# Performance work log

Hardware: AMD Instinct MI355X
Metric: run time of the kernel (lower is better)

Reference implementation:

```python
import jax, jax.numpy as jnp
import numpy as np

N_NODES = 100000
N_EDGES = 3200000
D = 256


def setup_inputs() -> dict:
    key = jax.random.key(0)
    ks = jax.random.split(key, 8)
    ego_embeddings = jax.random.normal(ks[0], (N_NODES, D), dtype=jnp.float32) * 0.1
    edge_vals = jax.random.uniform(ks[1], (N_EDGES,), dtype=jnp.float32) / 32.0  # ~normalized adjacency
    W1 = jax.random.normal(ks[2], (D, D), dtype=jnp.float32) * (1.0 / np.sqrt(D))
    b1 = jnp.zeros((D,), dtype=jnp.float32)
    W2 = jax.random.normal(ks[3], (D, D), dtype=jnp.float32) * (1.0 / np.sqrt(D))
    b2 = jnp.zeros((D,), dtype=jnp.float32)
    edge_rows = jax.random.randint(ks[4], (N_EDGES,), 0, N_NODES, dtype=jnp.int32)
    edge_cols = jax.random.randint(ks[5], (N_EDGES,), 0, N_NODES, dtype=jnp.int32)
    return {"ego_embeddings": ego_embeddings, "edge_vals": edge_vals,
            "W1": W1, "b1": b1, "W2": W2, "b2": b2,
            "edge_rows": edge_rows, "edge_cols": edge_cols}


def reference(ego_embeddings, edge_vals, W1, b1, W2, b2, edge_rows, edge_cols):
    # SpMM: side = A_in @ ego  (A_in in COO: rows, cols, vals)
    n = ego_embeddings.shape[0]
    gathered = ego_embeddings[edge_cols] * edge_vals[:, None]      # [E, D]
    side = jax.ops.segment_sum(gathered, edge_rows, num_segments=n)  # [N, D]
    # bi-interaction aggregator
    sum_emb = jax.nn.leaky_relu((ego_embeddings + side) @ W1.T + b1, negative_slope=0.01)
    bi_emb = jax.nn.leaky_relu((ego_embeddings * side) @ W2.T + b2, negative_slope=0.01)
    # dropout p=0.0 -> identity
    return sum_emb + bi_emb
```

## Files before the change

kernel.cpp:

```cpp
#include <hip/hip_runtime.h>
#include <hip/hip_fp16.h>
#include <stdint.h>

#define D 256
#define CHSH 13

typedef __attribute__((ext_vector_type(8))) short short8;
typedef __attribute__((ext_vector_type(4))) float floatx4;

__device__ __forceinline__ ushort f2bf(float f) {
    union { float f; uint32_t u; } v; v.f = f;
    uint32_t u = v.u;
    u += 0x7fffu + ((u >> 16) & 1u);
    return (ushort)(u >> 16);
}
__device__ __forceinline__ float bf2f(ushort h) {
    union { uint32_t u; float f; } v; v.u = ((uint32_t)h) << 16;
    return v.f;
}


__global__ void k_hist(const int* __restrict__ er, const int* __restrict__ ec,
                       const float* __restrict__ ev,
                       int* __restrict__ bp, uint64_t* __restrict__ aux,
                       int E, int NCH) {
    int e = blockIdx.x * 256 + threadIdx.x;
    if (e >= E) return;
    int row = er[e];
    int col = ec[e];
    int b = row * NCH + (col >> CHSH);
    atomicAdd(&bp[b], 1);
    ushort hb = __half_as_ushort(__float2half_rn(ev[e]));
    uint32_t payload = ((uint32_t)col << 15) | (uint32_t)hb;
    aux[e] = ((uint64_t)(uint32_t)b << 32) | payload;
}

__global__ void k_red(const int* __restrict__ bp, int* __restrict__ part, int nb) {
    __shared__ int s[256];
    int t = threadIdx.x;
    int base = blockIdx.x * 1024 + t * 4;
    int v = 0;
#pragma unroll
    for (int j = 0; j < 4; ++j) if (base + j < nb) v += bp[base + j];
    s[t] = v; __syncthreads();
    for (int off = 128; off; off >>= 1) {
        if (t < off) s[t] += s[t + off];
        __syncthreads();
    }
    if (t == 0) part[blockIdx.x] = s[0];
}

__global__ __launch_bounds__(1024) void k_scanpart(int* __restrict__ part, int np) {
    __shared__ int s[1024];
    int t = threadIdx.x;
    int p0 = (2 * t < np) ? part[2 * t] : 0;
    int p1 = (2 * t + 1 < np) ? part[2 * t + 1] : 0;
    int v = p0 + p1;
    s[t] = v; __syncthreads();
    for (int off = 1; off < 1024; off <<= 1) {
        int x = (t >= off) ? s[t - off] : 0;
        __syncthreads();
        s[t] += x;
        __syncthreads();
    }
    int excl = s[t] - v;
    if (2 * t < np) part[2 * t] = excl;
    if (2 * t + 1 < np) part[2 * t + 1] = excl + p0;
}

__global__ void k_scan3(int* __restrict__ bp, const int* __restrict__ part, int nb) {
    __shared__ int s[256];
    int t = threadIdx.x;
    int base = blockIdx.x * 1024 + t * 4;
    int d0 = 0, d1 = 0, d2 = 0, d3 = 0;
    if (base     < nb) d0 = bp[base];
    if (base + 1 < nb) d1 = bp[base + 1];
    if (base + 2 < nb) d2 = bp[base + 2];
    if (base + 3 < nb) d3 = bp[base + 3];
    int sum = d0 + d1 + d2 + d3;
    s[t] = sum; __syncthreads();
    for (int off = 1; off < 256; off <<= 1) {
        int x = (t >= off) ? s[t - off] : 0;
        __syncthreads();
        s[t] += x;
        __syncthreads();
    }
    int run = part[blockIdx.x] + s[t] - sum;
    if (base     < nb) bp[base]     = run; run += d0;
    if (base + 1 < nb) bp[base + 1] = run; run += d1;
    if (base + 2 < nb) bp[base + 2] = run; run += d2;
    if (base + 3 < nb) bp[base + 3] = run;
}

__global__ void k_scatter(const uint64_t* __restrict__ aux,
                          int* __restrict__ bp, uint32_t* __restrict__ csr,
                          int E, int BW) {
    int xcd = blockIdx.x & 7;
    int j = blockIdx.x >> 3;
    int e = j * 256 + threadIdx.x;
    if (e >= E) return;
    uint64_t a = aux[e];
    int b = (int)(a >> 32);
    int lo = xcd * BW;
    if (b < lo || b >= lo + BW) return;
    int p = atomicAdd(&bp[b], 1);
    csr[p] = (uint32_t)a;
}

__global__ void k_cvt(const float4* __restrict__ ego, ushort4* __restrict__ ego_bf,
                      const float4* __restrict__ W1, const float4* __restrict__ W2,
                      ushort4* __restrict__ W1b, ushort4* __restrict__ W2b, int n4) {
    int i = blockIdx.x * 256 + threadIdx.x;
    const float4* src;
    ushort4* dst;
    if (i < n4) { src = ego + i; dst = ego_bf + i; }
    else {
        int j = i - n4;
        if (j >= 32768) return;
        int k = j & 16383;
        src = ((j < 16384) ? W1 : W2) + k;
        dst = ((j < 16384) ? W1b : W2b) + k;
    }
    float4 f = *src;
    ushort4 u;
    u.x = f2bf(f.x); u.y = f2bf(f.y); u.z = f2bf(f.z); u.w = f2bf(f.w);
    *dst = u;
}

__global__ void k_spmm(const ushort* __restrict__ ego_bf, const int* __restrict__ bp,
                       const uint32_t* __restrict__ csr,
                       ushort* __restrict__ X1, ushort* __restrict__ X2, int n, int NCH) {
    int gtid = blockIdx.x * 256 + threadIdx.x;
    int node = gtid >> 6;
    int lane = gtid & 63;
    if (node >= n) return;
    int beg = (node == 0) ? 0 : bp[node * NCH - 1];
    int end = bp[(node + 1) * NCH - 1];
    int d0 = lane * 4;
    float a0 = 0.f, a1 = 0.f, a2 = 0.f, a3 = 0.f;
    int e = beg;
    for (; e + 8 <= end; e += 8) {
        uint32_t w[8];
#pragma unroll
        for (int j = 0; j < 8; ++j) w[j] = csr[e + j];
        ushort4 u[8];
#pragma unroll
        for (int j = 0; j < 8; ++j)
            u[j] = *(const ushort4*)(ego_bf + (size_t)(w[j] >> 15) * D + d0);
#pragma unroll
        for (int j = 0; j < 8; ++j) {
            float v = __half2float(__ushort_as_half((ushort)(w[j] & 0x7fff)));
            a0 += v * bf2f(u[j].x);
            a1 += v * bf2f(u[j].y);
            a2 += v * bf2f(u[j].z);
            a3 += v * bf2f(u[j].w);
        }
    }
    for (; e < end; ++e) {
        uint32_t w = csr[e];
        float v = __half2float(__ushort_as_half((ushort)(w & 0x7fff)));
        ushort4 u = *(const ushort4*)(ego_bf + (size_t)(w >> 15) * D + d0);
        a0 += v * bf2f(u.x);
        a1 += v * bf2f(u.y);
        a2 += v * bf2f(u.z);
        a3 += v * bf2f(u.w);
    }
    ushort4 eg = *(const ushort4*)(ego_bf + (size_t)node * D + d0);
    float e0 = bf2f(eg.x), e1 = bf2f(eg.y), e2 = bf2f(eg.z), e3 = bf2f(eg.w);
    ushort4 o1, o2;
    o1.x = f2bf(e0 + a0); o2.x = f2bf(e0 * a0);
    o1.y = f2bf(e1 + a1); o2.y = f2bf(e1 * a1);
    o1.z = f2bf(e2 + a2); o2.z = f2bf(e2 * a2);
    o1.w = f2bf(e3 + a3); o2.w = f2bf(e3 * a3);
    *(ushort4*)(X1 + (size_t)node * D + d0) = o1;
    *(ushort4*)(X2 + (size_t)node * D + d0) = o2;
}

__global__ __launch_bounds__(256) void k_gemm(
        const ushort* __restrict__ X1, const ushort* __restrict__ X2,
        const ushort* __restrict__ W1b, const ushort* __restrict__ W2b,
        const float* __restrict__ b1, const float* __restrict__ b2,
        float* __restrict__ out, int n) {
    int lane = threadIdx.x & 63;
    int w = threadIdx.x >> 6;
    int l16 = lane & 15, quad = lane >> 4;
    int row0 = blockIdx.x * 64;
    int colw = w * 64;

    floatx4 acc1[4][4], acc2[4][4];
#pragma unroll
    for (int i = 0; i < 4; ++i)
#pragma unroll
        for (int j = 0; j < 4; ++j) { acc1[i][j] = (floatx4)0.f; acc2[i][j] = (floatx4)0.f; }

    for (int kk = 0; kk < D; kk += 32) {
        short8 a[4], b[4];
#pragma unroll
        for (int mt = 0; mt < 4; ++mt)
            a[mt] = *(const short8*)(X1 + (size_t)(row0 + mt * 16 + l16) * D + kk + quad * 8);
#pragma unroll
        for (int nt = 0; nt < 4; ++nt)
            b[nt] = *(const short8*)(W1b + (size_t)(colw + nt * 16 + l16) * D + kk + quad * 8);
#pragma unroll
        for (int mt = 0; mt < 4; ++mt)
#pragma unroll
            for (int nt = 0; nt < 4; ++nt)
                acc1[mt][nt] = __builtin_amdgcn_mfma_f32_16x16x32_bf16(a[mt], b[nt], acc1[mt][nt], 0, 0, 0);
    }
    for (int kk = 0; kk < D; kk += 32) {
        short8 a[4], b[4];
#pragma unroll
        for (int mt = 0; mt < 4; ++mt)
            a[mt] = *(const short8*)(X2 + (size_t)(row0 + mt * 16 + l16) * D + kk + quad * 8);
#pragma unroll
        for (int nt = 0; nt < 4; ++nt)
            b[nt] = *(const short8*)(W2b + (size_t)(colw + nt * 16 + l16) * D + kk + quad * 8);
#pragma unroll
        for (int mt = 0; mt < 4; ++mt)
#pragma unroll
            for (int nt = 0; nt < 4; ++nt)
                acc2[mt][nt] = __builtin_amdgcn_mfma_f32_16x16x32_bf16(a[mt], b[nt], acc2[mt][nt], 0, 0, 0);
    }

#pragma unroll
    for (int nt = 0; nt < 4; ++nt) {
        int col = colw + nt * 16 + l16;
        float bb1 = b1[col], bb2 = b2[col];
#pragma unroll
        for (int mt = 0; mt < 4; ++mt) {
            int row = row0 + mt * 16 + quad * 4;
#pragma unroll
            for (int r = 0; r < 4; ++r) {
                if (row + r < n) {
                    float v1 = acc1[mt][nt][r] + bb1;
                    v1 = v1 > 0.f ? v1 : 0.01f * v1;
                    float v2 = acc2[mt][nt][r] + bb2;
                    v2 = v2 > 0.f ? v2 : 0.01f * v2;
                    out[(size_t)(row + r) * D + col] = v1 + v2;
                }
            }
        }
    }
}

extern "C" void kernel_launch(void* const* d_in, const int* in_sizes, int n_in,
                              void* d_out, int out_size, void* d_ws, size_t ws_size,
                              hipStream_t stream) {
    const float* ego   = (const float*)d_in[0];
    const float* evals = (const float*)d_in[1];
    const float* W1    = (const float*)d_in[2];
    const float* b1    = (const float*)d_in[3];
    const float* W2    = (const float*)d_in[4];
    const float* b2    = (const float*)d_in[5];
    const int* erows   = (const int*)d_in[6];
    const int* ecols   = (const int*)d_in[7];
    float* out = (float*)d_out;

    int n = in_sizes[0] / D;
    int E = in_sizes[1];
    int npad = (n + 63) & ~63;
    int NCH = (n + (1 << CHSH) - 1) >> CHSH;
    int nb = n * NCH;
    int np = (nb + 1023) / 1024;
    int BW = (nb + 7) / 8;

    char* p = (char*)d_ws;
    auto alloc = [&](size_t bytes) {
        char* q = p;
        p += (bytes + 511) & ~(size_t)511;
        return q;
    };
    ushort* ego_bf = (ushort*)alloc((size_t)n * D * 2);
    ushort* X1     = (ushort*)alloc((size_t)npad * D * 2);
    ushort* X2     = (ushort*)alloc((size_t)npad * D * 2);
    ushort* W1b    = (ushort*)alloc((size_t)D * D * 2);
    ushort* W2b    = (ushort*)alloc((size_t)D * D * 2);
    int* bp        = (int*)alloc((size_t)nb * 4);
    int* part      = (int*)alloc((size_t)np * 4);
    uint32_t* csr  = (uint32_t*)alloc((size_t)E * 4);

    uint64_t* aux = (uint64_t*)X1;

    hipMemsetAsync(bp, 0, (size_t)nb * 4, stream);
    int EB = (E + 255) / 256;
    k_hist<<<EB, 256, 0, stream>>>(erows, ecols, evals, bp, aux, E, NCH);
    k_red<<<np, 256, 0, stream>>>(bp, part, nb);
    k_scanpart<<<1, 1024, 0, stream>>>(part, np);
    k_scan3<<<np, 256, 0, stream>>>(bp, part, nb);
    k_scatter<<<8 * EB, 256, 0, stream>>>(aux, bp, csr, E, BW);

    int n4 = n * (D / 4);
    k_cvt<<<(n4 + 32768 + 255) / 256, 256, 0, stream>>>((const float4*)ego, (ushort4*)ego_bf,
                                                        (const float4*)W1, (const float4*)W2,
                                                        (ushort4*)W1b, (ushort4*)W2b, n4);

    k_spmm<<<(n * 64 + 255) / 256, 256, 0, stream>>>(ego_bf, bp, csr, X1, X2, n, NCH);

    k_gemm<<<npad / 64, 256, 0, stream>>>(X1, X2, W1b, W2b, b1, b2, out, n);
}
```

Before: 833.3 us.

## Process 25 nodes per wave in SpMM, iterating column chunks for gather locality

Each wavefront now owns 25 consecutive nodes and loops over column chunks outermost, accumulating every node's partial sums in registers. Within a chunk, all of those nodes gather from the same bounded column range, so the embedding rows they read are more likely to hit in cache. The cost is far fewer waves, roughly 100 accumulator registers per lane, a shallower 2-way unroll, and many small per-chunk loops that may cut memory-level parallelism.

```diff
diff --git a/kernel.cpp b/kernel.cpp
--- a/kernel.cpp
+++ b/kernel.cpp
@@ -4,6 +4,7 @@
 
 #define D 256
 #define CHSH 13
+#define NPW 25
 
 typedef __attribute__((ext_vector_type(8))) short short8;
 typedef __attribute__((ext_vector_type(4))) float floatx4;
@@ -127,53 +128,68 @@
     *dst = u;
 }
 
-__global__ void k_spmm(const ushort* __restrict__ ego_bf, const int* __restrict__ bp,
-                       const uint32_t* __restrict__ csr,
-                       ushort* __restrict__ X1, ushort* __restrict__ X2, int n, int NCH) {
-    int gtid = blockIdx.x * 256 + threadIdx.x;
-    int node = gtid >> 6;
-    int lane = gtid & 63;
-    if (node >= n) return;
-    int beg = (node == 0) ? 0 : bp[node * NCH - 1];
-    int end = bp[(node + 1) * NCH - 1];
+__global__ __launch_bounds__(256, 4) void k_spmm(
+        const ushort* __restrict__ ego_bf, const int* __restrict__ bp,
+        const uint32_t* __restrict__ csr,
+        ushort* __restrict__ X1, ushort* __restrict__ X2, int n, int NCH) {
+    int wid = __builtin_amdgcn_readfirstlane(blockIdx.x * 4 + (threadIdx.x >> 6));
+    int lane = threadIdx.x & 63;
+    int node0 = wid * NPW;
+    if (node0 >= n) return;
     int d0 = lane * 4;
-    float a0 = 0.f, a1 = 0.f, a2 = 0.f, a3 = 0.f;
-    int e = beg;
-    for (; e + 8 <= end; e += 8) {
-        uint32_t w[8];
-#pragma unroll
-        for (int j = 0; j < 8; ++j) w[j] = csr[e + j];
-        ushort4 u[8];
-#pragma unroll
-        for (int j = 0; j < 8; ++j)
-            u[j] = *(const ushort4*)(ego_bf + (size_t)(w[j] >> 15) * D + d0);
-#pragma unroll
-        for (int j = 0; j < 8; ++j) {
-            float v = __half2float(__ushort_as_half((ushort)(w[j] & 0x7fff)));
-            a0 += v * bf2f(u[j].x);
-            a1 += v * bf2f(u[j].y);
-            a2 += v * bf2f(u[j].z);
-            a3 += v * bf2f(u[j].w);
+
+    float acc[NPW][4];
+#pragma unroll
+    for (int i = 0; i < NPW; ++i) {
+        acc[i][0] = 0.f; acc[i][1] = 0.f; acc[i][2] = 0.f; acc[i][3] = 0.f;
+    }
+
+    for (int c = 0; c < NCH; ++c) {
+#pragma unroll
+        for (int i = 0; i < NPW; ++i) {
+            int node = node0 + i;
+            if (node < n) {
+                int idx = node * NCH + c;
+                int beg = (idx == 0) ? 0 : bp[idx - 1];
+                int end = bp[idx];
+                int e = beg;
+                for (; e + 2 <= end; e += 2) {
+                    uint32_t w0 = csr[e], w1 = csr[e + 1];
+                    ushort4 u0 = *(const ushort4*)(ego_bf + (size_t)(w0 >> 15) * D + d0);
+                    ushort4 u1 = *(const ushort4*)(ego_bf + (size_t)(w1 >> 15) * D + d0);
+                    float v0 = __half2float(__ushort_as_half((ushort)(w0 & 0x7fff)));
+                    float v1 = __half2float(__ushort_as_half((ushort)(w1 & 0x7fff)));
+                    acc[i][0] += v0 * bf2f(u0.x); acc[i][1] += v0 * bf2f(u0.y);
+                    acc[i][2] += v0 * bf2f(u0.z); acc[i][3] += v0 * bf2f(u0.w);
+                    acc[i][0] += v1 * bf2f(u1.x); acc[i][1] += v1 * bf2f(u1.y);
+                    acc[i][2] += v1 * bf2f(u1.z); acc[i][3] += v1 * bf2f(u1.w);
+                }
+                if (e < end) {
+                    uint32_t w = csr[e];
+                    float v = __half2float(__ushort_as_half((ushort)(w & 0x7fff)));
+                    ushort4 u = *(const ushort4*)(ego_bf + (size_t)(w >> 15) * D + d0);
+                    acc[i][0] += v * bf2f(u.x); acc[i][1] += v * bf2f(u.y);
+                    acc[i][2] += v * bf2f(u.z); acc[i][3] += v * bf2f(u.w);
+                }
+            }
         }
     }
-    for (; e < end; ++e) {
-        uint32_t w = csr[e];
-        float v = __half2float(__ushort_as_half((ushort)(w & 0x7fff)));
-        ushort4 u = *(const ushort4*)(ego_bf + (size_t)(w >> 15) * D + d0);
-        a0 += v * bf2f(u.x);
-        a1 += v * bf2f(u.y);
-        a2 += v * bf2f(u.z);
-        a3 += v * bf2f(u.w);
-    }
-    ushort4 eg = *(const ushort4*)(ego_bf + (size_t)node * D + d0);
-    float e0 = bf2f(eg.x), e1 = bf2f(eg.y), e2 = bf2f(eg.z), e3 = bf2f(eg.w);
-    ushort4 o1, o2;
-    o1.x = f2bf(e0 + a0); o2.x = f2bf(e0 * a0);
-    o1.y = f2bf(e1 + a1); o2.y = f2bf(e1 * a1);
-    o1.z = f2bf(e2 + a2); o2.z = f2bf(e2 * a2);
-    o1.w = f2bf(e3 + a3); o2.w = f2bf(e3 * a3);
-    *(ushort4*)(X1 + (size_t)node * D + d0) = o1;
-    *(ushort4*)(X2 + (size_t)node * D + d0) = o2;
+
+#pragma unroll
+    for (int i = 0; i < NPW; ++i) {
+        int node = node0 + i;
+        if (node < n) {
+            ushort4 eg = *(const ushort4*)(ego_bf + (size_t)node * D + d0);
+            float e0 = bf2f(eg.x), e1 = bf2f(eg.y), e2 = bf2f(eg.z), e3 = bf2f(eg.w);
+            ushort4 o1, o2;
+            o1.x = f2bf(e0 + acc[i][0]); o2.x = f2bf(e0 * acc[i][0]);
+            o1.y = f2bf(e1 + acc[i][1]); o2.y = f2bf(e1 * acc[i][1]);
+            o1.z = f2bf(e2 + acc[i][2]); o2.z = f2bf(e2 * acc[i][2]);
+            o1.w = f2bf(e3 + acc[i][3]); o2.w = f2bf(e3 * acc[i][3]);
+            *(ushort4*)(X1 + (size_t)node * D + d0) = o1;
+            *(ushort4*)(X2 + (size_t)node * D + d0) = o2;
+        }
+    }
 }
 
 __global__ __launch_bounds__(256) void k_gemm(
@@ -294,7 +310,9 @@
                                                         (const float4*)W1, (const float4*)W2,
                                                         (ushort4*)W1b, (ushort4*)W2b, n4);
 
-    k_spmm<<<(n * 64 + 255) / 256, 256, 0, stream>>>(ego_bf, bp, csr, X1, X2, n, NCH);
+    int nwaves = (n + NPW - 1) / NPW;
+    int nblocks = (nwaves + 3) / 4;
+    k_spmm<<<nblocks, 256, 0, stream>>>(ego_bf, bp, csr, X1, X2, n, NCH);
 
     k_gemm<<<npad / 64, 256, 0, stream>>>(X1, X2, W1b, W2b, b1, b2, out, n);
 }
```

New measurement: 965.7 us. +15.9%, slower.
